# Performance work log

Hardware: AMD Instinct MI355X
Metric: run time of the kernel (lower is better)

## Reference

```python
import jax, jax.numpy as jnp
import numpy as np

# Expansion with irrep_in = 128x0e+64x1e, irrep_out_1 = irrep_out_2 = 16x0e+8x1e
N0, N1 = 128, 64      # multiplicities of 0e / 1e in irrep_in
M0, M1 = 16, 8        # multiplicities of 0e / 1e in irrep_out_1 and irrep_out_2
B = 100000            # number of node pairs
SQRT3 = float(np.sqrt(3.0))
SQRT6 = float(np.sqrt(6.0))

# weight slice sizes per instruction (order: [0,0,0],[0,1,1],[1,0,1],[1,1,0],[1,1,1])
_S = [N0*M0*M0, N0*M1*M1, N1*M0*M1, N1*M1*M0, N1*M1*M1]
_OFF = np.cumsum([0] + _S)
NUM_PATH_WEIGHT = int(_OFF[-1])  # 61440

def _levi_civita():
    e = np.zeros((3, 3, 3), np.float32)
    e[0, 1, 2] = e[1, 2, 0] = e[2, 0, 1] = 1.0
    e[0, 2, 1] = e[2, 1, 0] = e[1, 0, 2] = -1.0
    return jnp.asarray(e)

EPS = _levi_civita()  # wigner_3j(1,1,1) = eps / sqrt(6) (up to e3nn global sign)

def setup_inputs() -> dict:
    key = jax.random.key(0)
    k1, k2 = jax.random.split(key)
    x_in = jax.random.normal(k1, (B, N0 + 3 * N1), dtype=jnp.float32)
    weights = jax.random.uniform(k2, (NUM_PATH_WEIGHT,), dtype=jnp.float32)
    return {"x_in": x_in, "weights": weights}

def reference(x_in, weights):
    Bn = x_in.shape[0]
    x0 = x_in[:, :N0]                      # [B, 128]  (0e channels)
    x1 = x_in[:, N0:].reshape(Bn, N1, 3)   # [B, 64, 3] (1e channels)

    w000 = weights[_OFF[0]:_OFF[1]].reshape(N0, M0, M0)
    w011 = weights[_OFF[1]:_OFF[2]].reshape(N0, M1, M1)
    w101 = weights[_OFF[2]:_OFF[3]].reshape(N1, M0, M1)
    w110 = weights[_OFF[3]:_OFF[4]].reshape(N1, M1, M0)
    w111 = weights[_OFF[4]:_OFF[5]].reshape(N1, M1, M1)

    eye3 = jnp.eye(3, dtype=x_in.dtype)

    # ins [0,0,0]: w3j(0,0,0)=1 -> block (0e,0e): [B, M0, M0]
    blk00 = jnp.einsum('wuv,bw->buv', w000, x0) / N0

    # ins [0,1,1]: w3j(1,1,0)=delta_ij/sqrt3 -> block (1e,1e): [B, M1,3, M1,3]
    r011 = jnp.einsum('wuv,bw->buv', w011, x0) / (N0 * SQRT3)
    blk11 = jnp.einsum('buv,ij->buivj', r011, eye3)

    # ins [1,1,1]: w3j(1,1,1)=eps/sqrt6 -> adds to block (1e,1e)
    blk11 = blk11 + jnp.einsum('wuv,ijk,bwk->buivj', w111, EPS, x1) / (N1 * SQRT6)
    blk11 = blk11.reshape(Bn, M1 * 3, M1 * 3)

    # ins [1,0,1]: w3j(0,1,1)=delta_jk/sqrt3 -> block (0e,1e): [B, M0, M1*3]
    blk01 = (jnp.einsum('wuv,bwj->buvj', w101, x1) / (N1 * SQRT3)).reshape(Bn, M0, M1 * 3)

    # ins [1,1,0]: w3j(1,0,1)=delta_ik/sqrt3 -> block (1e,0e): [B, M1*3, M0]
    blk10 = (jnp.einsum('wuv,bwi->buiv', w110, x1) / (N1 * SQRT3)).reshape(Bn, M1 * 3, M0)

    top = jnp.concatenate([blk00, blk01], axis=-1)   # [B, 16, 40]
    bot = jnp.concatenate([blk10, blk11], axis=-1)   # [B, 24, 40]
    return jnp.concatenate([top, bot], axis=-2)      # [B, 40, 40]
```

## Files before the change

kernel.cpp:

```cpp
#include <hip/hip_runtime.h>
#include <hip/hip_bf16.h>


typedef short bf16x8 __attribute__((ext_vector_type(8)));
typedef float f32x4 __attribute__((ext_vector_type(4)));

#define LGKM_BARRIER()                                         \
    do {                                                       \
        asm volatile("s_waitcnt lgkmcnt(0)" ::: "memory");     \
        __builtin_amdgcn_sched_barrier(0);                     \
        __builtin_amdgcn_s_barrier();                          \
        __builtin_amdgcn_sched_barrier(0);                     \
    } while (0)

static __device__ __forceinline__ unsigned short f2bf(float f) {
    __hip_bfloat16 h = __float2bfloat16(f);
    union { __hip_bfloat16 h; unsigned short u; } cvt; cvt.h = h;
    return cvt.u;
}

__global__ void prep_w(const float* __restrict__ w,
                       unsigned short* __restrict__ w0t,
                       unsigned short* __restrict__ w1t) {
    int idx = blockIdx.x * 256 + threadIdx.x;
    const float S000 = 1.0f / 128.0f;
    const float S011 = 1.0f / (128.0f * 1.7320508075688772f);
    const float S1X  = 1.0f / (64.0f * 1.7320508075688772f);
    const float S111 = 1.0f / (64.0f * 2.449489742783178f);
    if (idx < 320 * 128) {
        int n = idx >> 7, k = idx & 127;
        float v;
        if (n < 256) v = w[k * 256 + n] * S000;
        else         v = w[32768 + k * 64 + (n - 256)] * S011;
        w0t[idx] = f2bf(v);
    } else {
        int i2 = idx - 320 * 128;
        int n = i2 >> 6, k = i2 & 63;
        float v;
        if (n < 128)      v = w[40960 + k * 128 + n] * S1X;
        else if (n < 256) v = w[49152 + k * 128 + (n - 128)] * S1X;
        else              v = w[57344 + k * 64  + (n - 256)] * S111;
        w1t[i2] = f2bf(v);
    }
}

#define GRID 512

__global__ __launch_bounds__(256) void qhnet_main(
    const float* __restrict__ x_in,
    const unsigned short* __restrict__ w0t,
    const unsigned short* __restrict__ w1t,
    float* __restrict__ out,
    int ntiles)
{
    __shared__ __attribute__((aligned(16))) float smemf[8 * 1600];
    __shared__ __attribute__((aligned(16))) unsigned short xbuf[2][16 * 320];

    const int tid = threadIdx.x;
    const int lane = tid & 63;
    const int wv = tid >> 6;
    const int cn = lane & 15;
    const int grp = lane >> 4;
    const int swf = (cn & 7) << 3;
    const int rbase = (grp & 1) * 4;

    const int c0base[5] = {wv * 64, wv * 64 + 16, wv * 64 + 32, wv * 64 + 48,
                           256 + wv * 16};
    const int c1base[5] = {wv * 32, wv * 32 + 16, 128 + wv * 32,
                           128 + wv * 32 + 16, 256 + wv * 16};

    int s_row[5], s_col[5];
    #pragma unroll
    for (int k = 0; k < 5; ++k) {
        int p = tid + (k << 8);
        s_row[k] = p / 80;
        s_col[k] = (p - s_row[k] * 80) * 4;
    }

    int t = blockIdx.x;
    {
        const f32x4* xrow = reinterpret_cast<const f32x4*>(x_in + (size_t)t * 16 * 320);
        #pragma unroll
        for (int k = 0; k < 5; ++k) {
            f32x4 v = __builtin_nontemporal_load(&xrow[tid + (k << 8)]);
            int row = s_row[k], col = s_col[k], sw = (row & 7) << 3;
            if (col < 128) {
                ushort4 u;
                u.x = f2bf(v[0]); u.y = f2bf(v[1]); u.z = f2bf(v[2]); u.w = f2bf(v[3]);
                *reinterpret_cast<ushort4*>(&xbuf[0][row * 128 + (col ^ sw)]) = u;
            } else {
                #pragma unroll
                for (int e = 0; e < 4; ++e) {
                    int f = col - 128 + e;
                    int wi = f / 3, cm = f - wi * 3;
                    xbuf[0][2048 + cm * 1024 + row * 64 + (wi ^ sw)] = f2bf(v[e]);
                }
            }
        }
    }
    LGKM_BARRIER();

    int cur = 0;
    for (; t < ntiles; t += GRID) {
        const int b0 = t * 16;

        bf16x8 a0[4], a1[3][2];
        {
            const unsigned short* x0L = &xbuf[cur][0];
            const unsigned short* x1L = &xbuf[cur][2048];
            #pragma unroll
            for (int ks = 0; ks < 4; ++ks)
                a0[ks] = *reinterpret_cast<const bf16x8*>(
                    &x0L[cn * 128 + ((ks * 32 + grp * 8) ^ swf)]);
            #pragma unroll
            for (int c = 0; c < 3; ++c)
                #pragma unroll
                for (int ks = 0; ks < 2; ++ks)
                    a1[c][ks] = *reinterpret_cast<const bf16x8*>(
                        &x1L[c * 1024 + cn * 64 + ((ks * 32 + grp * 8) ^ swf)]);
        }

        const bool more = (t + GRID) < ntiles;
        f32x4 v[5];
        if (more) {
            const f32x4* xrow = reinterpret_cast<const f32x4*>(
                x_in + (size_t)(t + GRID) * 16 * 320);
            #pragma unroll
            for (int k = 0; k < 5; ++k)
                v[k] = __builtin_nontemporal_load(&xrow[tid + (k << 8)]);
        }

        f32x4 acc0[5] = {};
        f32x4 acc1[3][5] = {};
        #pragma unroll
        for (int tt = 0; tt < 5; ++tt) {
            const unsigned short* wp = w0t + (c0base[tt] + cn) * 128 + grp * 8;
            #pragma unroll
            for (int ks = 0; ks < 4; ++ks) {
                bf16x8 b = *reinterpret_cast<const bf16x8*>(wp + ks * 32);
                acc0[tt] = __builtin_amdgcn_mfma_f32_16x16x32_bf16(a0[ks], b, acc0[tt], 0, 0, 0);
            }
        }
        #pragma unroll
        for (int tt = 0; tt < 5; ++tt) {
            const unsigned short* wp = w1t + (c1base[tt] + cn) * 64 + grp * 8;
            #pragma unroll
            for (int ks = 0; ks < 2; ++ks) {
                bf16x8 b = *reinterpret_cast<const bf16x8*>(wp + ks * 32);
                #pragma unroll
                for (int c = 0; c < 3; ++c)
                    acc1[c][tt] = __builtin_amdgcn_mfma_f32_16x16x32_bf16(a1[c][ks], b, acc1[c][tt], 0, 0, 0);
            }
        }

        if (more) {
            const int nb = cur ^ 1;
            #pragma unroll
            for (int k = 0; k < 5; ++k) {
                int row = s_row[k], col = s_col[k], sw = (row & 7) << 3;
                if (col < 128) {
                    ushort4 u;
                    u.x = f2bf(v[k][0]); u.y = f2bf(v[k][1]);
                    u.z = f2bf(v[k][2]); u.w = f2bf(v[k][3]);
                    *reinterpret_cast<ushort4*>(&xbuf[nb][row * 128 + (col ^ sw)]) = u;
                } else {
                    #pragma unroll
                    for (int e = 0; e < 4; ++e) {
                        int f = col - 128 + e;
                        int wi = f / 3, cm = f - wi * 3;
                        xbuf[nb][2048 + cm * 1024 + row * 64 + (wi ^ sw)] = f2bf(v[k][e]);
                    }
                }
            }
        }
        LGKM_BARRIER();

        #pragma unroll
        for (int h = 0; h < 2; ++h) {
            if (h) LGKM_BARRIER();
            if ((grp >> 1) == h) {
                #pragma unroll
                for (int tt = 0; tt < 4; ++tt) {
                    int u = wv * 4 + tt;
                    #pragma unroll
                    for (int r = 0; r < 4; ++r)
                        smemf[(rbase + r) * 1600 + u * 40 + cn] = acc0[tt][r];
                }
                #pragma unroll
                for (int tt = 0; tt < 2; ++tt) {
                    int n01 = wv * 32 + tt * 16 + cn;
                    int u01 = n01 >> 3, v01 = n01 & 7;
                    int u10 = n01 >> 4, v10 = n01 & 15;
                    #pragma unroll
                    for (int r = 0; r < 4; ++r) {
                        float* o01 = &smemf[(rbase + r) * 1600 + u01 * 40 + 16 + 3 * v01];
                        o01[0] = acc1[0][tt][r];
                        o01[1] = acc1[1][tt][r];
                        o01[2] = acc1[2][tt][r];
                        #pragma unroll
                        for (int c = 0; c < 3; ++c)
                            smemf[(rbase + r) * 1600 + (16 + 3 * u10 + c) * 40 + v10] = acc1[c][tt + 2][r];
                    }
                }
                {
                    int uv = wv * 16 + cn, u = uv >> 3, vv2 = uv & 7;
                    #pragma unroll
                    for (int r = 0; r < 4; ++r) {
                        float d  = acc0[4][r];
                        float t0 = acc1[0][4][r], t1 = acc1[1][4][r], t2 = acc1[2][4][r];
                        float* o = &smemf[(rbase + r) * 1600 + (16 + 3 * u) * 40 + 16 + 3 * vv2];
                        o[0]  = d;    o[1]  = t2;   o[2]  = -t1;
                        o[40] = -t2;  o[41] = d;    o[42] = t0;
                        o[80] = t1;   o[81] = -t0;  o[82] = d;
                    }
                }
            }
            LGKM_BARRIER();
            float* dstf = out + (size_t)(b0 + h * 8) * 1600;
            const f32x4* srcv = reinterpret_cast<const f32x4*>(smemf);
            #pragma unroll
            for (int k = 0; k < 13; ++k) {
                int p = tid + (k << 8);
                if (k < 12 || tid < 128) {
                    f32x4 val = srcv[p];
                    __builtin_nontemporal_store(
                        val, reinterpret_cast<f32x4*>(dstf + (size_t)p * 4));
                }
            }
        }
        cur ^= 1;
    }
}

extern "C" void kernel_launch(void* const* d_in, const int* in_sizes, int n_in,
                              void* d_out, int out_size, void* d_ws, size_t ws_size,
                              hipStream_t stream) {
    const float* x_in = (const float*)d_in[0];
    const float* weights = (const float*)d_in[1];
    float* out = (float*)d_out;
    unsigned short* w0t = (unsigned short*)d_ws;
    unsigned short* w1t = w0t + 320 * 128;
    int B = in_sizes[0] / 320;

    prep_w<<<240, 256, 0, stream>>>(weights, w0t, w1t);
    qhnet_main<<<GRID, 256, 0, stream>>>(x_in, w0t, w1t, out, B / 16);
}
```

Measured before the change: 165.1 us.

## Transpose MFMA operands for vectorized LDS staging, shrink smem, raise grid

Swaps the MFMA A/B operands so each lane's accumulator holds four consecutive output columns for one batch row. The epilogue can then write whole float4 quads into a smaller 4-row LDS staging buffer with an XOR swizzle, replacing scalar scattered stores. The epilogue now runs in four barrier-separated phases instead of two. The halved shared memory allows more blocks per CU, and the grid is raised to 768 to use them. The cost is extra barriers and index arithmetic in the readback.

Result: slower. 174.3 us (+5.6%).

```diff
diff --git a/kernel.cpp b/kernel.cpp
--- a/kernel.cpp
+++ b/kernel.cpp
@@ -44,7 +44,7 @@
     }
 }
 
-#define GRID 512
+#define GRID 768
 
 __global__ __launch_bounds__(256) void qhnet_main(
     const float* __restrict__ x_in,
@@ -53,8 +53,9 @@
     float* __restrict__ out,
     int ntiles)
 {
-    __shared__ __attribute__((aligned(16))) float smemf[8 * 1600];
+    __shared__ __attribute__((aligned(16))) float smemf[4 * 1600];
     __shared__ __attribute__((aligned(16))) unsigned short xbuf[2][16 * 320];
+    f32x4* smemq = reinterpret_cast<f32x4*>(smemf);
 
     const int tid = threadIdx.x;
     const int lane = tid & 63;
@@ -62,7 +63,9 @@
     const int cn = lane & 15;
     const int grp = lane >> 4;
     const int swf = (cn & 7) << 3;
-    const int rbase = (grp & 1) * 4;
+    const int g2 = grp >> 1, g1 = grp & 1;
+    const int tr = cn & 3;
+    f32x4* rowq = smemq + tr * 400;
 
     const int c0base[5] = {wv * 64, wv * 64 + 16, wv * 64 + 32, wv * 64 + 48,
                            256 + wv * 16};
@@ -138,7 +141,7 @@
             #pragma unroll
             for (int ks = 0; ks < 4; ++ks) {
                 bf16x8 b = *reinterpret_cast<const bf16x8*>(wp + ks * 32);
-                acc0[tt] = __builtin_amdgcn_mfma_f32_16x16x32_bf16(a0[ks], b, acc0[tt], 0, 0, 0);
+                acc0[tt] = __builtin_amdgcn_mfma_f32_16x16x32_bf16(b, a0[ks], acc0[tt], 0, 0, 0);
             }
         }
         #pragma unroll
@@ -149,7 +152,7 @@
                 bf16x8 b = *reinterpret_cast<const bf16x8*>(wp + ks * 32);
                 #pragma unroll
                 for (int c = 0; c < 3; ++c)
-                    acc1[c][tt] = __builtin_amdgcn_mfma_f32_16x16x32_bf16(a1[c][ks], b, acc1[c][tt], 0, 0, 0);
+                    acc1[c][tt] = __builtin_amdgcn_mfma_f32_16x16x32_bf16(b, a1[c][ks], acc1[c][tt], 0, 0, 0);
             }
         }
 
@@ -176,53 +179,68 @@
         LGKM_BARRIER();
 
         #pragma unroll
-        for (int h = 0; h < 2; ++h) {
+        for (int h = 0; h < 4; ++h) {
             if (h) LGKM_BARRIER();
-            if ((grp >> 1) == h) {
+            if ((cn >> 2) == h) {
                 #pragma unroll
                 for (int tt = 0; tt < 4; ++tt) {
-                    int u = wv * 4 + tt;
+                    int q = (wv * 4 + tt) * 10 + grp;
+                    rowq[q ^ tr] = acc0[tt];
+                }
+                #pragma unroll
+                for (int tt = 0; tt < 2; ++tt) {
+                    int u01 = 4 * wv + 2 * tt + g2;
+                    int q0 = u01 * 10 + 4 + 3 * g1;
+                    f32x4 qa = {acc1[0][tt][0], acc1[1][tt][0], acc1[2][tt][0], acc1[0][tt][1]};
+                    f32x4 qb = {acc1[1][tt][1], acc1[2][tt][1], acc1[0][tt][2], acc1[1][tt][2]};
+                    f32x4 qc = {acc1[2][tt][2], acc1[0][tt][3], acc1[1][tt][3], acc1[2][tt][3]};
+                    rowq[q0 ^ tr]       = qa;
+                    rowq[(q0 + 1) ^ tr] = qb;
+                    rowq[(q0 + 2) ^ tr] = qc;
+                }
+                #pragma unroll
+                for (int tt = 0; tt < 2; ++tt) {
+                    int rr = 16 + 3 * (2 * wv + tt);
                     #pragma unroll
-                    for (int r = 0; r < 4; ++r)
-                        smemf[(rbase + r) * 1600 + u * 40 + cn] = acc0[tt][r];
-                }
-                #pragma unroll
-                for (int tt = 0; tt < 2; ++tt) {
-                    int n01 = wv * 32 + tt * 16 + cn;
-                    int u01 = n01 >> 3, v01 = n01 & 7;
-                    int u10 = n01 >> 4, v10 = n01 & 15;
-                    #pragma unroll
-                    for (int r = 0; r < 4; ++r) {
-                        float* o01 = &smemf[(rbase + r) * 1600 + u01 * 40 + 16 + 3 * v01];
-                        o01[0] = acc1[0][tt][r];
-                        o01[1] = acc1[1][tt][r];
-                        o01[2] = acc1[2][tt][r];
-                        #pragma unroll
-                        for (int c = 0; c < 3; ++c)
-                            smemf[(rbase + r) * 1600 + (16 + 3 * u10 + c) * 40 + v10] = acc1[c][tt + 2][r];
+                    for (int c = 0; c < 3; ++c) {
+                        int q = (rr + c) * 10 + grp;
+                        rowq[q ^ tr] = acc1[c][tt + 2];
                     }
                 }
                 {
-                    int uv = wv * 16 + cn, u = uv >> 3, vv2 = uv & 7;
-                    #pragma unroll
-                    for (int r = 0; r < 4; ++r) {
-                        float d  = acc0[4][r];
-                        float t0 = acc1[0][4][r], t1 = acc1[1][4][r], t2 = acc1[2][4][r];
-                        float* o = &smemf[(rbase + r) * 1600 + (16 + 3 * u) * 40 + 16 + 3 * vv2];
-                        o[0]  = d;    o[1]  = t2;   o[2]  = -t1;
-                        o[40] = -t2;  o[41] = d;    o[42] = t0;
-                        o[80] = t1;   o[81] = -t0;  o[82] = d;
-                    }
+                    int rr = 16 + 3 * (2 * wv + g2);
+                    int cq = 4 + 3 * g1;
+                    f32x4 d = acc0[4];
+                    f32x4 t0 = acc1[0][4], t1 = acc1[1][4], t2 = acc1[2][4];
+                    f32x4 q00 = {d[0], t2[0], -t1[0], d[1]};
+                    f32x4 q01 = {t2[1], -t1[1], d[2], t2[2]};
+                    f32x4 q02 = {-t1[2], d[3], t2[3], -t1[3]};
+                    f32x4 q10 = {-t2[0], d[0], t0[0], -t2[1]};
+                    f32x4 q11 = {d[1], t0[1], -t2[2], d[2]};
+                    f32x4 q12 = {t0[2], -t2[3], d[3], t0[3]};
+                    f32x4 q20 = {t1[0], -t0[0], d[0], t1[1]};
+                    f32x4 q21 = {-t0[1], d[1], t1[2], -t0[2]};
+                    f32x4 q22 = {d[2], t1[3], -t0[3], d[3]};
+                    rowq[(rr * 10 + cq)            ^ tr] = q00;
+                    rowq[(rr * 10 + cq + 1)        ^ tr] = q01;
+                    rowq[(rr * 10 + cq + 2)        ^ tr] = q02;
+                    rowq[((rr + 1) * 10 + cq)      ^ tr] = q10;
+                    rowq[((rr + 1) * 10 + cq + 1)  ^ tr] = q11;
+                    rowq[((rr + 1) * 10 + cq + 2)  ^ tr] = q12;
+                    rowq[((rr + 2) * 10 + cq)      ^ tr] = q20;
+                    rowq[((rr + 2) * 10 + cq + 1)  ^ tr] = q21;
+                    rowq[((rr + 2) * 10 + cq + 2)  ^ tr] = q22;
                 }
             }
             LGKM_BARRIER();
-            float* dstf = out + (size_t)(b0 + h * 8) * 1600;
-            const f32x4* srcv = reinterpret_cast<const f32x4*>(smemf);
-            #pragma unroll
-            for (int k = 0; k < 13; ++k) {
+            float* dstf = out + (size_t)(b0 + h * 4) * 1600;
+            #pragma unroll
+            for (int k = 0; k < 7; ++k) {
                 int p = tid + (k << 8);
-                if (k < 12 || tid < 128) {
-                    f32x4 val = srcv[p];
+                if (k < 6 || tid < 64) {
+                    int row = p / 400;
+                    int q = p - row * 400;
+                    f32x4 val = smemq[row * 400 + (q ^ row)];
                     __builtin_nontemporal_store(
                         val, reinterpret_cast<f32x4*>(dstf + (size_t)p * 4));
                 }
```
